# Kernel tuning notes

Hardware: AMD Instinct MI355X
Metric: run time of the kernel (lower is better)

Reference implementation:

```python
import jax, jax.numpy as jnp
import numpy as np

N = 50000
E = 800000

def _glorot(k, shape):
    lim = float(np.sqrt(6.0 / (shape[0] + shape[1])))
    return jax.random.uniform(k, shape, jnp.float32, -lim, lim)

def setup_inputs() -> dict:
    key = jax.random.key(0)
    ks = jax.random.split(key, 12)
    x = jax.random.normal(ks[0], (N, 58), jnp.float32)
    edge_index = jax.random.randint(ks[1], (2, E), 0, N, jnp.int32)
    neg_edge_index = jax.random.randint(ks[2], (2, E), 0, N, jnp.int32)
    return dict(
        x=x, edge_index=edge_index, neg_edge_index=neg_edge_index,
        W1_0=_glorot(ks[3], (58, 300)), W1_1=_glorot(ks[4], (58, 300)), b1=jnp.zeros((300,), jnp.float32),
        W2_0=_glorot(ks[5], (300, 100)), W2_1=_glorot(ks[6], (300, 100)), b2=jnp.zeros((100,), jnp.float32),
        W3_0=_glorot(ks[7], (100, 1)), W3_1=_glorot(ks[8], (100, 1)), b3=jnp.zeros((1,), jnp.float32),
        lin1_W=_glorot(ks[9], (100, 58)), lin1_b=jnp.zeros((100,), jnp.float32),
        lin2_W=_glorot(ks[10], (100, 58)), lin2_b=jnp.zeros((100,), jnp.float32),
        c1=jnp.full((1,), 0.5, jnp.float32), c2=jnp.full((1,), 0.5, jnp.float32),
    )

def _cheb(x, src, dst, norm, W0, W1, b):
    tx1 = jax.ops.segment_sum(x[src] * norm[:, None], dst, num_segments=x.shape[0])
    return x @ W0 + tx1 @ W1 + b

def reference(x, edge_index, neg_edge_index,
              W1_0, W1_1, b1, W2_0, W2_1, b2, W3_0, W3_1, b3,
              lin1_W, lin1_b, lin2_W, lin2_b, c1, c2):
    src, dst = edge_index[0], edge_index[1]
    deg = jax.ops.segment_sum(jnp.ones((E,), x.dtype), src, num_segments=N)
    dis = jnp.where(deg > 0, 1.0 / jnp.sqrt(jnp.where(deg > 0, deg, 1.0)), 0.0)
    norm = -(dis[src] * dis[dst])  # [E]
    h = jax.nn.relu(_cheb(x, src, dst, norm, W1_0, W1_1, b1))      # [N,300]
    x1 = jax.nn.relu(_cheb(h, src, dst, norm, W2_0, W2_1, b2))     # [N,100]
    xm = x1 + jax.nn.relu(x @ lin1_W.T + lin1_b)
    z = x1 + jax.nn.relu(x @ lin2_W.T + lin2_b)
    pos_score = jnp.sum(z[edge_index[0]] * z[edge_index[1]], axis=1)
    pos_loss = -jnp.mean(jnp.log(jax.nn.sigmoid(pos_score) + 1e-15))
    neg_score = jnp.sum(z[neg_edge_index[0]] * z[neg_edge_index[1]], axis=1)
    neg_loss = -jnp.mean(jnp.log(1.0 - jax.nn.sigmoid(neg_score) + 1e-15))
    r_loss = pos_loss + neg_loss
    out = _cheb(xm, src, dst, norm, W3_0, W3_1, b3)                # [N,1]
    return (out, r_loss, c1, c2)
```

## Files before the change

kernel.cpp:

```cpp
#include <hip/hip_runtime.h>
#include <math.h>

#define NN 50000
#define NE 800000
#define SB2 2048
#define LB 1024
#define CAP 64

using bf16x8 = __attribute__((ext_vector_type(8))) short;
using f32x4  = __attribute__((ext_vector_type(4))) float;
using f32x2  = __attribute__((ext_vector_type(2))) float;
using i32x8  = __attribute__((ext_vector_type(8))) int;

__device__ __forceinline__ float b2f(short s) {
    union { unsigned u; float f; } v;
    v.u = ((unsigned)(unsigned short)s) << 16;
    return v.f;
}
__device__ __forceinline__ unsigned short f2b(float f) {
    union { float f; unsigned u; } v;
    v.f = f;
    unsigned r = v.u + 0x7fffu + ((v.u >> 16) & 1u);
    return (unsigned short)(r >> 16);
}
__device__ __forceinline__ unsigned char f2e4m3(float f) {
    return (unsigned char)(__builtin_amdgcn_cvt_pk_fp8_f32(f, f, 0, false) & 0xff);
}
__device__ __forceinline__ void acc8(float* acc, uint2 u) {
    f32x2 p0 = __builtin_amdgcn_cvt_pk_f32_fp8(u.x, false);
    f32x2 p1 = __builtin_amdgcn_cvt_pk_f32_fp8(u.x, true);
    f32x2 p2 = __builtin_amdgcn_cvt_pk_f32_fp8(u.y, false);
    f32x2 p3 = __builtin_amdgcn_cvt_pk_f32_fp8(u.y, true);
    acc[0] += p0.x; acc[1] += p0.y;
    acc[2] += p1.x; acc[3] += p1.y;
    acc[4] += p2.x; acc[5] += p2.y;
    acc[6] += p3.x; acc[7] += p3.y;
}

__global__ void k_build(const int* __restrict__ ei, int* __restrict__ degs,
                        int* __restrict__ cnt, unsigned short* __restrict__ bkt16) {
    int e = blockIdx.x * 256 + threadIdx.x;
    if (e < NE) {
        int s = ei[e], d = ei[NE + e];
        atomicAdd(&degs[s], 1);
        int slot = atomicAdd(&cnt[d], 1);
        if (slot < CAP) bkt16[(d << 6) + slot] = (unsigned short)s;
    }
}

__global__ __launch_bounds__(256) void k_prep(const float* __restrict__ x,
                                              unsigned short* __restrict__ xcat,
                                              unsigned char* __restrict__ xf8,
                                              const int* __restrict__ degs,
                                              float* __restrict__ dis,
                                              const float* __restrict__ W1_0,
                                              const float* __restrict__ W1_1,
                                              const float* __restrict__ W2_0,
                                              const float* __restrict__ W2_1,
                                              const float* __restrict__ L1,
                                              const float* __restrict__ L2,
                                              unsigned short* __restrict__ Wt1f,
                                              unsigned short* __restrict__ Wt2f,
                                              unsigned short* __restrict__ Wtlf) {
    int b = blockIdx.x;
    if (b < 12500) {
        int t = b * 256 + threadIdx.x;
        int n = t >> 6, k = t & 63;
        float v = (k < 58) ? x[(size_t)n * 58 + k] : 0.0f;
        xcat[(size_t)n * 128 + k] = f2b(v);
        int dg = degs[n];
        float dv = dg > 0 ? 1.0f / sqrtf((float)dg) : 0.0f;
        xf8[(size_t)n * 64 + k] = f2e4m3(dv * v);
        return;
    }
    if (b < 12696) {
        int i = (b - 12500) * 256 + threadIdx.x;
        if (i < NN) {
            int dg = degs[i];
            dis[i] = dg > 0 ? 1.0f / sqrtf((float)dg) : 0.0f;
        }
        return;
    }
    int t = (b - 12696) * 256 + threadIdx.x;
    if (t < 40960) {
        int f = t >> 9, lane = (t >> 3) & 63, j = t & 7;
        int nt = f >> 2, s = f & 3;
        int ml = lane & 15, quad = lane >> 4;
        int k = s * 32 + quad * 8 + j;
        int col = nt * 16 + ml;
        float v = 0.0f;
        if (col < 300) {
            if (k < 58) v = W1_0[k * 300 + col];
            else if (k >= 64 && k < 122) v = W1_1[(k - 64) * 300 + col];
        }
        Wt1f[t] = f2b(v);
    } else if (t < 107520) {
        int u = t - 40960;
        int f = u >> 9, lane = (u >> 3) & 63, j = u & 7;
        int nt = f / 10, s = f - nt * 10;
        int ml = lane & 15, quad = lane >> 4;
        int k = s * 32 + quad * 8 + j;
        int col = nt * 16 + ml;
        float v = 0.0f;
        if (k < 300) {
            if (col < 100) v = W2_0[k * 100 + col];
            else if (col >= 104 && col < 204) v = W2_1[k * 100 + (col - 104)];
        }
        Wt2f[u] = f2b(v);
    } else if (t < 120832) {
        int u = t - 107520;
        int f = u >> 9, lane = (u >> 3) & 63, j = u & 7;
        int nt = f >> 1, s = f & 1;
        int ml = lane & 15, quad = lane >> 4;
        int k = s * 32 + quad * 8 + j;
        int col = nt * 16 + ml;
        float v = 0.0f;
        if (k < 58) {
            if (col < 100) v = L1[col * 58 + k];
            else if (col >= 104 && col < 204) v = L2[(col - 104) * 58 + k];
        }
        Wtlf[u] = f2b(v);
    }
}

__global__ __launch_bounds__(256) void k_gather58(const int* __restrict__ cnt,
                                                  const unsigned short* __restrict__ bkt16,
                                                  const float* __restrict__ dis,
                                                  const unsigned char* __restrict__ xf8,
                                                  unsigned short* __restrict__ xcat) {
    int t = blockIdx.x * 256 + threadIdx.x;
    int n = t >> 3, l = t & 7;
    if (n >= NN) return;
    int c = cnt[n]; if (c > CAP) c = CAP;
    float dn = dis[n];
    const unsigned short* bp = bkt16 + (n << 6);
    float acc[8] = {0, 0, 0, 0, 0, 0, 0, 0};
    for (int i = 0; i < c; i++) {
        unsigned src = bp[i];
        uint2 u = *(const uint2*)(xf8 + (size_t)src * 64 + l * 8);
        acc8(acc, u);
    }
    bf16x8 o;
#pragma unroll
    for (int j = 0; j < 8; j++) o[j] = (short)f2b(-dn * acc[j]);
    *(bf16x8*)(xcat + (size_t)n * 128 + 64 + l * 8) = o;
}

__global__ __launch_bounds__(256) void k_mm12(const unsigned short* __restrict__ xcat,
                                              const unsigned short* __restrict__ Wt1f,
                                              const float* __restrict__ b1,
                                              const unsigned short* __restrict__ Wt2f,
                                              const float* __restrict__ dis,
                                              float* __restrict__ hp,
                                              unsigned char* __restrict__ hwf8) {
    __shared__ __attribute__((aligned(16))) unsigned short hs[64 * 328];
    __shared__ __attribute__((aligned(16))) unsigned short bst[2][5120];
    int tid = threadIdx.x;
    int wave = tid >> 6, lane = tid & 63, ml = lane & 15, quad = lane >> 4;
    int row0 = blockIdx.x * 64;
    int rw = row0 + wave * 16;

    int ar = rw + ml; if (ar >= NN) ar = NN - 1;
    const bf16x8* Ap = (const bf16x8*)(xcat + (size_t)ar * 128 + quad * 8);
    bf16x8 a0 = Ap[0], a1 = Ap[4], a2 = Ap[8], a3 = Ap[12];
    float dv[4];
#pragma unroll
    for (int r = 0; r < 4; r++) {
        int row = rw + quad * 4 + r;
        dv[r] = dis[row < NN ? row : NN - 1];
    }

    ((bf16x8*)bst[0])[tid] = ((const bf16x8*)Wt1f)[tid];
    __syncthreads();

    for (int nt = 0; nt < 20; nt++) {
        if (nt + 1 < 20)
            ((bf16x8*)bst[(nt + 1) & 1])[tid] =
                ((const bf16x8*)(Wt1f + (size_t)(nt + 1) * 2048))[tid];
        const bf16x8* Bp = (const bf16x8*)bst[nt & 1];
        f32x4 acc = {0.f, 0.f, 0.f, 0.f};
        acc = __builtin_amdgcn_mfma_f32_16x16x32_bf16(a0, Bp[0 * 64 + lane], acc, 0, 0, 0);
        acc = __builtin_amdgcn_mfma_f32_16x16x32_bf16(a1, Bp[1 * 64 + lane], acc, 0, 0, 0);
        acc = __builtin_amdgcn_mfma_f32_16x16x32_bf16(a2, Bp[2 * 64 + lane], acc, 0, 0, 0);
        acc = __builtin_amdgcn_mfma_f32_16x16x32_bf16(a3, Bp[3 * 64 + lane], acc, 0, 0, 0);
        int col = nt * 16 + ml;
        float bias = (col < 300) ? b1[col] : 0.0f;
#pragma unroll
        for (int r = 0; r < 4; r++) {
            float v = acc[r] + bias;
            v = v > 0.0f ? v : 0.0f;
            if (col >= 300) v = 0.0f;
            hs[(wave * 16 + quad * 4 + r) * 328 + col] = f2b(v);
        }
        __syncthreads();
    }

    for (int i = tid; i < 640; i += 256)
        ((bf16x8*)bst[0])[i] = ((const bf16x8*)Wt2f)[i];
    bf16x8 A2[10];
#pragma unroll
    for (int s = 0; s < 10; s++)
        A2[s] = *(const bf16x8*)(hs + (wave * 16 + ml) * 328 + s * 32 + quad * 8);
    __syncthreads();

    for (int nt = 0; nt < 13; nt++) {
        if (nt + 1 < 13)
            for (int i = tid; i < 640; i += 256)
                ((bf16x8*)bst[(nt + 1) & 1])[i] =
                    ((const bf16x8*)(Wt2f + (size_t)(nt + 1) * 5120))[i];
        const bf16x8* Bp = (const bf16x8*)bst[nt & 1];
        f32x4 acc = {0.f, 0.f, 0.f, 0.f};
#pragma unroll
        for (int s = 0; s < 10; s++)
            acc = __builtin_amdgcn_mfma_f32_16x16x32_bf16(A2[s], Bp[s * 64 + lane], acc, 0, 0, 0);
        int j = nt * 16 + ml;
#pragma unroll
        for (int r = 0; r < 4; r++) {
            int row = rw + quad * 4 + r;
            if (row < NN) {
                if (j < 104) hp[(size_t)row * 104 + j] = acc[r];
                else hwf8[(size_t)row * 128 + (j - 104)] = f2e4m3(dv[r] * acc[r]);
            }
        }
        __syncthreads();
    }
}

__global__ __launch_bounds__(256) void k_gather100(const int* __restrict__ cnt,
                                                   const unsigned short* __restrict__ bkt16,
                                                   const float* __restrict__ dis,
                                                   const unsigned char* __restrict__ hwf8,
                                                   float* __restrict__ tx2) {
    int t = blockIdx.x * 256 + threadIdx.x;
    int n = t >> 4, l = t & 15;
    if (n >= NN || l >= 13) return;
    int c = cnt[n]; if (c > CAP) c = CAP;
    float dn = dis[n];
    const unsigned short* bp = bkt16 + (n << 6);
    float acc[8] = {0, 0, 0, 0, 0, 0, 0, 0};
    for (int i = 0; i < c; i++) {
        unsigned src = bp[i];
        uint2 u = *(const uint2*)(hwf8 + (size_t)src * 128 + l * 8);
        acc8(acc, u);
    }
    f32x4 o0 = {-dn * acc[0], -dn * acc[1], -dn * acc[2], -dn * acc[3]};
    f32x4 o1 = {-dn * acc[4], -dn * acc[5], -dn * acc[6], -dn * acc[7]};
    *(f32x4*)(tx2 + (size_t)n * 104 + l * 8) = o0;
    *(f32x4*)(tx2 + (size_t)n * 104 + l * 8 + 4) = o1;
}

__global__ __launch_bounds__(256) void k_mmlin3(const unsigned short* __restrict__ xcat,
                                                const unsigned short* __restrict__ Wtlf,
                                                const float* __restrict__ hp,
                                                const float* __restrict__ tx2,
                                                const float* __restrict__ dis,
                                                const float* __restrict__ b2,
                                                const float* __restrict__ l1b,
                                                const float* __restrict__ l2b,
                                                const float* __restrict__ W30,
                                                const float* __restrict__ W31,
                                                const float* __restrict__ b3,
                                                float* __restrict__ out,
                                                float* __restrict__ qbuf,
                                                unsigned char* __restrict__ zf8) {
    int tid = threadIdx.x;
    int wave = tid >> 6, lane = tid & 63, ml = lane & 15, quad = lane >> 4;
    int row0 = blockIdx.x * 64;
    int rw = row0 + wave * 16;
    if (rw >= NN) return;

    int ar = rw + ml; if (ar >= NN) ar = NN - 1;
    const bf16x8* Ap = (const bf16x8*)(xcat + (size_t)ar * 128 + quad * 8);
    bf16x8 a0 = Ap[0], a1 = Ap[4];
    float p0[4] = {0, 0, 0, 0}, p1[4] = {0, 0, 0, 0};
    float b3v = b3[0];

    for (int nt = 0; nt < 13; nt++) {
        bf16x8 bw0 = *(const bf16x8*)(Wtlf + (size_t)((nt * 2 + 0) * 64 + lane) * 8);
        bf16x8 bw1 = *(const bf16x8*)(Wtlf + (size_t)((nt * 2 + 1) * 64 + lane) * 8);
        f32x4 acc = {0.f, 0.f, 0.f, 0.f};
        acc = __builtin_amdgcn_mfma_f32_16x16x32_bf16(a0, bw0, acc, 0, 0, 0);
        acc = __builtin_amdgcn_mfma_f32_16x16x32_bf16(a1, bw1, acc, 0, 0, 0);
        int j = nt * 16 + ml;
        int jj = (j < 104) ? j : j - 104;
        float bb = 0.0f, lb = 0.0f;
        if (jj < 100) {
            bb = b2[jj];
            lb = (j < 104) ? l1b[jj] : l2b[jj];
        }
        float w0 = (j < 100) ? W30[j] : 0.0f;
        float w1 = (j < 100) ? W31[j] : 0.0f;
#pragma unroll
        for (int r = 0; r < 4; r++) {
            int row = rw + quad * 4 + r;
            int rcl = row < NN ? row : NN - 1;
            float x1v = hp[(size_t)rcl * 104 + jj] + tx2[(size_t)rcl * 104 + jj] + bb;
            x1v = x1v > 0.0f ? x1v : 0.0f;
            float lv = acc[r] + lb;
            lv = lv > 0.0f ? lv : 0.0f;
            float o = x1v + lv;
            if (j < 104) {
                p0[r] += o * w0;
                p1[r] += o * w1;
            } else if (row < NN) {
                zf8[(size_t)row * 128 + (j - 104)] = f2e4m3(o);
            }
        }
    }
#pragma unroll
    for (int m = 1; m < 16; m <<= 1) {
#pragma unroll
        for (int r = 0; r < 4; r++) {
            p0[r] += __shfl_xor(p0[r], m, 64);
            p1[r] += __shfl_xor(p1[r], m, 64);
        }
    }
    if (ml == 0) {
#pragma unroll
        for (int r = 0; r < 4; r++) {
            int row = rw + quad * 4 + r;
            if (row < NN) {
                out[row] = p0[r] + b3v;
                qbuf[row] = dis[row] * p1[r];
            }
        }
    }
    for (int idx = lane; idx < 16 * 6; idx += 64) {
        int rr = rw + idx / 6;
        if (rr < NN) *(unsigned*)(zf8 + (size_t)rr * 128 + 104 + (idx % 6) * 4) = 0u;
    }
}

__global__ __launch_bounds__(256) void k_score(const unsigned char* __restrict__ zf8,
                                               const int* __restrict__ ei,
                                               const int* __restrict__ nei,
                                               float* __restrict__ pbuf) {
    int lane = threadIdx.x & 63;
    int wid = (blockIdx.x * 256 + threadIdx.x) >> 6;
    int nw = SB2 * 4;
    int ml = lane & 15, quad = lane >> 4;
    int dr = ml - quad * 4;
    bool diag = (dr >= 0 && dr < 4);
    const int G = (2 * NE) / 16;
    for (int g = wid; g < G; g += nw) {
        int base = g * 16;
        int a, b;
        if (base < NE) {
            a = ei[base + ml];
            b = ei[NE + base + ml];
        } else {
            a = nei[base - NE + ml];
            b = nei[base + ml];
        }
        i32x8 av = *(const i32x8*)(zf8 + (size_t)a * 128 + quad * 32);
        i32x8 bv = *(const i32x8*)(zf8 + (size_t)b * 128 + quad * 32);
        f32x4 d = {0.f, 0.f, 0.f, 0.f};
        d = __builtin_amdgcn_mfma_scale_f32_16x16x128_f8f6f4(
                av, bv, d, 0, 0, 0, 0x7f7f7f7f, 0, 0x7f7f7f7f);
        if (diag) pbuf[base + ml] = d[dr];
    }
}

__global__ __launch_bounds__(256) void k_loss(const float* __restrict__ pbuf,
                                              double* __restrict__ red) {
    double acc = 0.0;
    for (int i = blockIdx.x * 256 + threadIdx.x; i < 2 * NE; i += LB * 256) {
        float p = pbuf[i];
        float sg = 1.0f / (1.0f + expf(-p));
        float term = (i < NE) ? logf(sg + 1e-15f) : logf(1.0f - sg + 1e-15f);
        acc += (double)term;
    }
    __shared__ double sred[256];
    sred[threadIdx.x] = acc;
    __syncthreads();
    for (int s = 128; s; s >>= 1) {
        if (threadIdx.x < s) sred[threadIdx.x] += sred[threadIdx.x + s];
        __syncthreads();
    }
    if (threadIdx.x == 0) red[blockIdx.x] = sred[0];
}

__global__ __launch_bounds__(256) void k_final_g1(const double* __restrict__ red,
                                                  const float* __restrict__ c1,
                                                  const float* __restrict__ c2,
                                                  const int* __restrict__ cnt,
                                                  const unsigned short* __restrict__ bkt16,
                                                  const float* __restrict__ dis,
                                                  const float* __restrict__ qbuf,
                                                  float* __restrict__ out) {
    if (blockIdx.x == 0) {
        double a = 0.0;
        for (int i = threadIdx.x; i < LB; i += 256) a += red[i];
        __shared__ double sred[256];
        sred[threadIdx.x] = a;
        __syncthreads();
        for (int st = 128; st; st >>= 1) {
            if (threadIdx.x < st) sred[threadIdx.x] += sred[threadIdx.x + st];
            __syncthreads();
        }
        if (threadIdx.x == 0) {
            out[NN] = (float)(-sred[0] / (double)NE);
            out[NN + 1] = c1[0];
            out[NN + 2] = c2[0];
        }
        return;
    }
    int n = (blockIdx.x - 1) * 256 + threadIdx.x;
    if (n >= NN) return;
    int c = cnt[n]; if (c > CAP) c = CAP;
    const unsigned short* bp = bkt16 + (n << 6);
    float acc = 0.0f;
    for (int i = 0; i < c; i++) acc += qbuf[bp[i]];
    out[n] += -dis[n] * acc;
}

extern "C" void kernel_launch(void* const* d_in, const int* in_sizes, int n_in,
                              void* d_out, int out_size, void* d_ws, size_t ws_size,
                              hipStream_t stream) {
    const float* x    = (const float*)d_in[0];
    const int*   ei   = (const int*)d_in[1];
    const int*   nei  = (const int*)d_in[2];
    const float* W1_0 = (const float*)d_in[3];
    const float* W1_1 = (const float*)d_in[4];
    const float* b1   = (const float*)d_in[5];
    const float* W2_0 = (const float*)d_in[6];
    const float* W2_1 = (const float*)d_in[7];
    const float* b2   = (const float*)d_in[8];
    const float* W3_0 = (const float*)d_in[9];
    const float* W3_1 = (const float*)d_in[10];
    const float* b3   = (const float*)d_in[11];
    const float* l1W  = (const float*)d_in[12];
    const float* l1b  = (const float*)d_in[13];
    const float* l2W  = (const float*)d_in[14];
    const float* l2b  = (const float*)d_in[15];
    const float* c1   = (const float*)d_in[16];
    const float* c2   = (const float*)d_in[17];
    float* out = (float*)d_out;
    float* w = (float*)d_ws;

    unsigned short* bkt16  = (unsigned short*)w;
    int*            degs   = (int*)(w + 1600000);
    int*            cnt    = (int*)(w + 1650000);
    float*          dis    = w + 1700000;
    float*          qbuf   = w + 1750000;
    double*         red    = (double*)(w + 1800000);
    float*          pbuf   = w + 1802048;
    unsigned short* xcat   = (unsigned short*)(w + 3402048);
    unsigned short* Wt1f   = (unsigned short*)(w + 6602048);
    unsigned short* Wt2f   = (unsigned short*)(w + 6622528);
    unsigned short* Wtlf   = (unsigned short*)(w + 6655808);
    float*          hp     = w + 6662464;
    unsigned char*  hwf8   = (unsigned char*)(w + 11862464);
    unsigned char*  zf8    = (unsigned char*)(w + 13462464);
    unsigned char*  xf8    = (unsigned char*)(w + 15062464);
    float*          tx2    = w + 15862464;

    hipMemsetAsync(degs, 0, 100000 * sizeof(int), stream);

    k_build<<<(NE + 255) / 256, 256, 0, stream>>>(ei, degs, cnt, bkt16);
    k_prep<<<13168, 256, 0, stream>>>(x, xcat, xf8, degs, dis,
                                      W1_0, W1_1, W2_0, W2_1, l1W, l2W,
                                      Wt1f, Wt2f, Wtlf);

    k_gather58<<<(NN * 8 + 255) / 256, 256, 0, stream>>>(cnt, bkt16, dis, xf8, xcat);
    k_mm12<<<(NN + 63) / 64, 256, 0, stream>>>(xcat, Wt1f, b1, Wt2f, dis, hp, hwf8);

    k_gather100<<<NN * 16 / 256, 256, 0, stream>>>(cnt, bkt16, dis, hwf8, tx2);
    k_mmlin3<<<(NN + 63) / 64, 256, 0, stream>>>(xcat, Wtlf, hp, tx2, dis,
                                                 b2, l1b, l2b, W3_0, W3_1, b3,
                                                 out, qbuf, zf8);

    k_score<<<SB2, 256, 0, stream>>>(zf8, ei, nei, pbuf);
    k_loss<<<LB, 256, 0, stream>>>(pbuf, red);
    k_final_g1<<<1 + (NN + 255) / 256, 256, 0, stream>>>(red, c1, c2, cnt, bkt16, dis, qbuf, out);
}
```

Measured before the change: 369.5 us.

## Fuse edge scoring, loss reduction and final gather into one tail kernel

Merges the score, loss and final-gather kernels into a single launch. Edge scores are computed with MFMA, redistributed across lanes with ds_bpermute and turned into log-sigmoid terms in registers, so the 6.4 MB pbuf round trip is gone. The global reduction now uses a double atomicAdd plus a last-block counter, so two launches and the partial-sum buffer are removed. Extra blocks in the same grid do the layer-3 gather. The per-thread accumulator changes from double to float, which may cost a little precision, and the atomics add some contention.

Result: slower. 445.5 us (+20.6%).

```diff
diff --git a/kernel.cpp b/kernel.cpp
--- a/kernel.cpp
+++ b/kernel.cpp
@@ -4,7 +4,7 @@
 #define NN 50000
 #define NE 800000
 #define SB2 2048
-#define LB 1024
+#define GB 196
 #define CAP 64
 
 using bf16x8 = __attribute__((ext_vector_type(8))) short;
@@ -331,87 +331,93 @@
     }
 }
 
-__global__ __launch_bounds__(256) void k_score(const unsigned char* __restrict__ zf8,
-                                               const int* __restrict__ ei,
-                                               const int* __restrict__ nei,
-                                               float* __restrict__ pbuf) {
-    int lane = threadIdx.x & 63;
-    int wid = (blockIdx.x * 256 + threadIdx.x) >> 6;
-    int nw = SB2 * 4;
+__global__ __launch_bounds__(256) void k_tail(const unsigned char* __restrict__ zf8,
+                                              const int* __restrict__ ei,
+                                              const int* __restrict__ nei,
+                                              const int* __restrict__ cnt,
+                                              const unsigned short* __restrict__ bkt16,
+                                              const float* __restrict__ dis,
+                                              const float* __restrict__ qbuf,
+                                              const float* __restrict__ c1,
+                                              const float* __restrict__ c2,
+                                              double* __restrict__ dred,
+                                              int* __restrict__ dcnt,
+                                              float* __restrict__ out) {
+    int tid = threadIdx.x;
+    if (blockIdx.x >= SB2) {
+        int n = (blockIdx.x - SB2) * 256 + tid;
+        if (n >= NN) return;
+        int c = cnt[n]; if (c > CAP) c = CAP;
+        const unsigned short* bp = bkt16 + (n << 6);
+        float acc = 0.0f;
+        for (int i = 0; i < c; i++) acc += qbuf[bp[i]];
+        out[n] += -dis[n] * acc;
+        return;
+    }
+    int lane = tid & 63;
+    int wv = (blockIdx.x * 256 + tid) >> 6;
+    const int NW = SB2 * 4;
     int ml = lane & 15, quad = lane >> 4;
     int dr = ml - quad * 4;
     bool diag = (dr >= 0 && dr < 4);
-    const int G = (2 * NE) / 16;
-    for (int g = wid; g < G; g += nw) {
-        int base = g * 16;
-        int a, b;
-        if (base < NE) {
-            a = ei[base + ml];
-            b = ei[NE + base + ml];
-        } else {
-            a = nei[base - NE + ml];
-            b = nei[base + ml];
-        }
-        i32x8 av = *(const i32x8*)(zf8 + (size_t)a * 128 + quad * 32);
-        i32x8 bv = *(const i32x8*)(zf8 + (size_t)b * 128 + quad * 32);
-        f32x4 d = {0.f, 0.f, 0.f, 0.f};
-        d = __builtin_amdgcn_mfma_scale_f32_16x16x128_f8f6f4(
-                av, bv, d, 0, 0, 0, 0x7f7f7f7f, 0, 0x7f7f7f7f);
-        if (diag) pbuf[base + ml] = d[dr];
-    }
-}
-
-__global__ __launch_bounds__(256) void k_loss(const float* __restrict__ pbuf,
-                                              double* __restrict__ red) {
-    double acc = 0.0;
-    for (int i = blockIdx.x * 256 + threadIdx.x; i < 2 * NE; i += LB * 256) {
-        float p = pbuf[i];
+    int dri = diag ? dr : 0;
+    int srck = lane & 15;
+    int srclane = 20 * (srck >> 2) + (srck & 3);
+    int baddr = srclane << 2;
+    int tsel = lane >> 4;
+    float facc = 0.0f;
+    const int NBATCH = (2 * NE) / 64;
+    for (int b = wv; b < NBATCH; b += NW) {
+        float sc[4];
+        unsigned pmask = 0;
+#pragma unroll
+        for (int t = 0; t < 4; t++) {
+            int base = b * 64 + t * 16;
+            int a, bb;
+            if (base < NE) {
+                a = ei[base + ml];
+                bb = ei[NE + base + ml];
+                pmask |= (1u << t);
+            } else {
+                a = nei[base - NE + ml];
+                bb = nei[base + ml];
+            }
+            i32x8 av = *(const i32x8*)(zf8 + (size_t)a * 128 + quad * 32);
+            i32x8 bv = *(const i32x8*)(zf8 + (size_t)bb * 128 + quad * 32);
+            f32x4 d = {0.f, 0.f, 0.f, 0.f};
+            d = __builtin_amdgcn_mfma_scale_f32_16x16x128_f8f6f4(
+                    av, bv, d, 0, 0, 0, 0x7f7f7f7f, 0, 0x7f7f7f7f);
+            sc[t] = d[dri];
+        }
+        int v0 = __builtin_amdgcn_ds_bpermute(baddr, __float_as_int(sc[0]));
+        int v1 = __builtin_amdgcn_ds_bpermute(baddr, __float_as_int(sc[1]));
+        int v2 = __builtin_amdgcn_ds_bpermute(baddr, __float_as_int(sc[2]));
+        int v3 = __builtin_amdgcn_ds_bpermute(baddr, __float_as_int(sc[3]));
+        int vi = (tsel == 0) ? v0 : (tsel == 1) ? v1 : (tsel == 2) ? v2 : v3;
+        float p = __int_as_float(vi);
+        bool pos = (pmask >> tsel) & 1;
         float sg = 1.0f / (1.0f + expf(-p));
-        float term = (i < NE) ? logf(sg + 1e-15f) : logf(1.0f - sg + 1e-15f);
-        acc += (double)term;
+        float term = pos ? logf(sg + 1e-15f) : logf(1.0f - sg + 1e-15f);
+        facc += term;
     }
     __shared__ double sred[256];
-    sred[threadIdx.x] = acc;
+    sred[tid] = (double)facc;
     __syncthreads();
     for (int s = 128; s; s >>= 1) {
-        if (threadIdx.x < s) sred[threadIdx.x] += sred[threadIdx.x + s];
+        if (tid < s) sred[tid] += sred[tid + s];
         __syncthreads();
     }
-    if (threadIdx.x == 0) red[blockIdx.x] = sred[0];
-}
-
-__global__ __launch_bounds__(256) void k_final_g1(const double* __restrict__ red,
-                                                  const float* __restrict__ c1,
-                                                  const float* __restrict__ c2,
-                                                  const int* __restrict__ cnt,
-                                                  const unsigned short* __restrict__ bkt16,
-                                                  const float* __restrict__ dis,
-                                                  const float* __restrict__ qbuf,
-                                                  float* __restrict__ out) {
-    if (blockIdx.x == 0) {
-        double a = 0.0;
-        for (int i = threadIdx.x; i < LB; i += 256) a += red[i];
-        __shared__ double sred[256];
-        sred[threadIdx.x] = a;
-        __syncthreads();
-        for (int st = 128; st; st >>= 1) {
-            if (threadIdx.x < st) sred[threadIdx.x] += sred[threadIdx.x + st];
-            __syncthreads();
-        }
-        if (threadIdx.x == 0) {
-            out[NN] = (float)(-sred[0] / (double)NE);
+    if (tid == 0) {
+        atomicAdd(dred, sred[0]);
+        __threadfence();
+        int old = atomicAdd(dcnt, 1);
+        if (old == SB2 - 1) {
+            double total = atomicAdd(dred, 0.0);
+            out[NN] = (float)(-total / (double)NE);
             out[NN + 1] = c1[0];
             out[NN + 2] = c2[0];
         }
-        return;
-    }
-    int n = (blockIdx.x - 1) * 256 + threadIdx.x;
-    if (n >= NN) return;
-    int c = cnt[n]; if (c > CAP) c = CAP;
-    const unsigned short* bp = bkt16 + (n << 6);
-    float acc = 0.0f;
-    for (int i = 0; i < c; i++) acc += qbuf[bp[i]];
-    out[n] += -dis[n] * acc;
+    }
 }
 
 extern "C" void kernel_launch(void* const* d_in, const int* in_sizes, int n_in,
@@ -441,21 +447,21 @@
     unsigned short* bkt16  = (unsigned short*)w;
     int*            degs   = (int*)(w + 1600000);
     int*            cnt    = (int*)(w + 1650000);
-    float*          dis    = w + 1700000;
-    float*          qbuf   = w + 1750000;
-    double*         red    = (double*)(w + 1800000);
-    float*          pbuf   = w + 1802048;
-    unsigned short* xcat   = (unsigned short*)(w + 3402048);
-    unsigned short* Wt1f   = (unsigned short*)(w + 6602048);
-    unsigned short* Wt2f   = (unsigned short*)(w + 6622528);
-    unsigned short* Wtlf   = (unsigned short*)(w + 6655808);
-    float*          hp     = w + 6662464;
-    unsigned char*  hwf8   = (unsigned char*)(w + 11862464);
-    unsigned char*  zf8    = (unsigned char*)(w + 13462464);
-    unsigned char*  xf8    = (unsigned char*)(w + 15062464);
-    float*          tx2    = w + 15862464;
-
-    hipMemsetAsync(degs, 0, 100000 * sizeof(int), stream);
+    double*         dred   = (double*)(w + 1700000);
+    int*            dcnt   = (int*)(w + 1700002);
+    float*          dis    = w + 1700008;
+    float*          qbuf   = w + 1750008;
+    unsigned short* xcat   = (unsigned short*)(w + 1800008);
+    unsigned short* Wt1f   = (unsigned short*)(w + 5000008);
+    unsigned short* Wt2f   = (unsigned short*)(w + 5020488);
+    unsigned short* Wtlf   = (unsigned short*)(w + 5053768);
+    float*          hp     = w + 5060424;
+    unsigned char*  hwf8   = (unsigned char*)(w + 10260424);
+    unsigned char*  zf8    = (unsigned char*)(w + 11860424);
+    unsigned char*  xf8    = (unsigned char*)(w + 13460424);
+    float*          tx2    = w + 14260424;
+
+    hipMemsetAsync(degs, 0, 100004 * sizeof(int), stream);
 
     k_build<<<(NE + 255) / 256, 256, 0, stream>>>(ei, degs, cnt, bkt16);
     k_prep<<<13168, 256, 0, stream>>>(x, xcat, xf8, degs, dis,
@@ -470,7 +476,6 @@
                                                  b2, l1b, l2b, W3_0, W3_1, b3,
                                                  out, qbuf, zf8);
 
-    k_score<<<SB2, 256, 0, stream>>>(zf8, ei, nei, pbuf);
-    k_loss<<<LB, 256, 0, stream>>>(pbuf, red);
-    k_final_g1<<<1 + (NN + 255) / 256, 256, 0, stream>>>(red, c1, c2, cnt, bkt16, dis, qbuf, out);
-}
+    k_tail<<<SB2 + GB, 256, 0, stream>>>(zf8, ei, nei, cnt, bkt16, dis, qbuf,
+                                         c1, c2, dred, dcnt, out);
+}
```
